# Performance work log

Hardware: AMD Instinct MI355X
Metric: run time of the kernel (lower is better)

The kernel has to match this reference:

```python
import jax, jax.numpy as jnp
import numpy as np

HIDDEN_DIM = 1024
NUM_HEADS = 16
HEAD_DIM = HIDDEN_DIM // NUM_HEADS
ROPE_BASE = 10000.0


def setup_inputs() -> dict:
    key = jax.random.key(0)
    kx, kq, kk, kv, ko = jax.random.split(key, 5)
    B, S = 2, 2048
    scale = 1.0 / np.sqrt(HIDDEN_DIM)
    x = jax.random.normal(kx, (B, S, HIDDEN_DIM), dtype=jnp.float32)
    Wq = jax.random.normal(kq, (HIDDEN_DIM, HIDDEN_DIM), dtype=jnp.float32) * scale
    Wk = jax.random.normal(kk, (HIDDEN_DIM, HIDDEN_DIM), dtype=jnp.float32) * scale
    Wv = jax.random.normal(kv, (HIDDEN_DIM, HIDDEN_DIM), dtype=jnp.float32) * scale
    Wo = jax.random.normal(ko, (HIDDEN_DIM, HIDDEN_DIM), dtype=jnp.float32) * scale
    return {"x": x, "Wq": Wq, "Wk": Wk, "Wv": Wv, "Wo": Wo}


def _apply_rope(t, positions):
    # t: (B, S, H, D), positions: (B, S)
    half = HEAD_DIM // 2
    inv_freq = 1.0 / (ROPE_BASE ** (jnp.arange(0, half, dtype=jnp.float32) * 2.0 / HEAD_DIM))
    freqs = positions[..., None].astype(jnp.float32) * inv_freq  # (B, S, D/2)
    emb = jnp.concatenate([freqs, freqs], axis=-1)  # (B, S, D)
    cos = jnp.cos(emb)[:, :, None, :]
    sin = jnp.sin(emb)[:, :, None, :]
    t1, t2 = t[..., :half], t[..., half:]
    rot = jnp.concatenate([-t2, t1], axis=-1)
    return t * cos + rot * sin


def reference(x, Wq, Wk, Wv, Wo):
    B, S, _ = x.shape
    H, D = NUM_HEADS, HEAD_DIM
    q = (x @ Wq.T).reshape(B, S, H, D)
    k = (x @ Wk.T).reshape(B, S, H, D)
    v = (x @ Wv.T).reshape(B, S, H, D)
    positions = jnp.broadcast_to(jnp.arange(S)[None, :], (B, S))
    q = _apply_rope(q, positions)
    k = _apply_rope(k, positions)
    # SDPA (non-causal, no mask): scores (B, H, S, S)
    scale = 1.0 / np.sqrt(D)
    scores = jnp.einsum('bqhd,bkhd->bhqk', q, k) * scale
    probs = jax.nn.softmax(scores, axis=-1)
    out = jnp.einsum('bhqk,bkhd->bqhd', probs, v).reshape(B, S, H * D)
    return out @ Wo.T
```

## Files before the change

kernel.cpp:

```cpp
#include <hip/hip_runtime.h>


typedef unsigned short u16;
typedef unsigned int   u32;
typedef __bf16 bf16x8 __attribute__((ext_vector_type(8)));
typedef float  f32x4  __attribute__((ext_vector_type(4)));
typedef u16    u16x8  __attribute__((ext_vector_type(8)));
typedef u16    u16x4  __attribute__((ext_vector_type(4)));
typedef u32    u32x4  __attribute__((ext_vector_type(4)));

#define HID 1024
#define SEQ 2048
#define NH  16
#define HD  64

#if __has_builtin(__builtin_amdgcn_exp2f)
#define EXP2F(x) __builtin_amdgcn_exp2f(x)
#else
#define EXP2F(x) exp2f(x)
#endif

__device__ __forceinline__ float bf2f(u16 u) { return __uint_as_float(((unsigned)u) << 16); }
__device__ __forceinline__ u16 f2bf(float f) {
  union { __bf16 h; u16 u; } c;
  c.h = (__bf16)f;
  return c.u;
}
__device__ __forceinline__ void gl_lds16(const void* g, void* l) {
  __builtin_amdgcn_global_load_lds((const __attribute__((address_space(1))) void*)g,
                                   (__attribute__((address_space(3))) void*)l, 16, 0, 0);
}
__device__ __forceinline__ void stage_f32(const float* __restrict__ src, u16* dst) {
  float4 f0 = *(const float4*)src;
  float4 f1 = *(const float4*)(src + 4);
  u16x8 o;
  o[0] = f2bf(f0.x); o[1] = f2bf(f0.y); o[2] = f2bf(f0.z); o[3] = f2bf(f0.w);
  o[4] = f2bf(f1.x); o[5] = f2bf(f1.y); o[6] = f2bf(f1.z); o[7] = f2bf(f1.w);
  *(u16x8*)dst = o;
}
__device__ __forceinline__ int swz(int c, int r) { return c ^ (r & 7); }

__global__ void cvt_pre(const float* __restrict__ x,  const float* __restrict__ Wq,
                        const float* __restrict__ Wk, const float* __restrict__ Wv,
                        u16* __restrict__ xb, u16* __restrict__ Wqb,
                        u16* __restrict__ Wkb, u16* __restrict__ Wvb) {
  const int z = blockIdx.y;
  const float* src; u16* dst; int nchunk;
  switch (z) {
    case 0:  src = x;  dst = xb;  nchunk = 524288; break;
    case 1:  src = Wq; dst = Wqb; nchunk = 131072; break;
    case 2:  src = Wk; dst = Wkb; nchunk = 131072; break;
    default: src = Wv; dst = Wvb; nchunk = 131072; break;
  }
  const int i = blockIdx.x * 256 + threadIdx.x;
  if (i >= nchunk) return;
  stage_f32(src + (size_t)i * 8, dst + (size_t)i * 8);
}
__global__ void cvt_wo(const float* __restrict__ Wo, u16* __restrict__ Wob) {
  const int i = blockIdx.x * 256 + threadIdx.x;
  stage_f32(Wo + (size_t)i * 8, Wob + (size_t)i * 8);
}

__device__ __forceinline__ void gemm_mainloop(const u16* __restrict__ Aptr,
                                              const u16* __restrict__ Bptr,
                                              u16* a_lds, u16* b_lds,
                                              int m0, int n0, f32x4 (&acc)[4][4]) {
  const int tid  = threadIdx.x;
  const int w    = tid >> 6;
  const int lane = tid & 63;
  const int quad = lane >> 4, l15 = lane & 15;
  const int wm = (w >> 1) * 64, wn = (w & 1) * 64;
  const int srow = lane >> 3, sc = lane & 7;

  for (int k0 = 0; k0 < HID; k0 += 64) {
#pragma unroll
    for (int i = 0; i < 4; ++i) {
      const int seg = w * 4 + i;
      const int r   = seg * 8 + srow;
      const int col = k0 + swz(sc, srow) * 8;
      gl_lds16(Aptr + (size_t)(m0 + r) * HID + col, a_lds + seg * 512);
      gl_lds16(Bptr + (size_t)(n0 + r) * HID + col, b_lds + seg * 512);
    }
    __syncthreads();
#pragma unroll
    for (int kf = 0; kf < 2; ++kf) {
      bf16x8 af[4], bfr[4];
#pragma unroll
      for (int mt = 0; mt < 4; ++mt)
        af[mt] = *(const bf16x8*)&a_lds[(wm + mt * 16 + l15) * 64 + swz(kf * 4 + quad, l15) * 8];
#pragma unroll
      for (int nt = 0; nt < 4; ++nt)
        bfr[nt] = *(const bf16x8*)&b_lds[(wn + nt * 16 + l15) * 64 + swz(kf * 4 + quad, l15) * 8];
#pragma unroll
      for (int mt = 0; mt < 4; ++mt)
#pragma unroll
        for (int nt = 0; nt < 4; ++nt)
          acc[mt][nt] = __builtin_amdgcn_mfma_f32_16x16x32_bf16(af[mt], bfr[nt], acc[mt][nt], 0, 0, 0);
    }
    __syncthreads();
  }
}

__device__ __forceinline__ void gemm64_mainloop(const u16* __restrict__ Aptr,
                                                const u16* __restrict__ Bptr,
                                                u16* a_lds, u16* b_lds,
                                                int m0, int n0, f32x4 (&acc)[2][4]) {
  const int tid  = threadIdx.x;
  const int w    = tid >> 6;
  const int lane = tid & 63;
  const int quad = lane >> 4, l15 = lane & 15;
  const int wm = (w >> 1) * 32, wn = (w & 1) * 64;
  const int srow = lane >> 3, sc = lane & 7;

  for (int k0 = 0; k0 < HID; k0 += 64) {
#pragma unroll
    for (int i = 0; i < 2; ++i) {
      const int seg = w * 2 + i, r = seg * 8 + srow;
      gl_lds16(Aptr + (size_t)(m0 + r) * HID + k0 + swz(sc, srow) * 8, a_lds + seg * 512);
    }
#pragma unroll
    for (int i = 0; i < 4; ++i) {
      const int seg = w * 4 + i, r = seg * 8 + srow;
      gl_lds16(Bptr + (size_t)(n0 + r) * HID + k0 + swz(sc, srow) * 8, b_lds + seg * 512);
    }
    __syncthreads();
#pragma unroll
    for (int kf = 0; kf < 2; ++kf) {
      bf16x8 af[2], bfr[4];
#pragma unroll
      for (int mt = 0; mt < 2; ++mt)
        af[mt] = *(const bf16x8*)&a_lds[(wm + mt * 16 + l15) * 64 + swz(kf * 4 + quad, l15) * 8];
#pragma unroll
      for (int nt = 0; nt < 4; ++nt)
        bfr[nt] = *(const bf16x8*)&b_lds[(wn + nt * 16 + l15) * 64 + swz(kf * 4 + quad, l15) * 8];
#pragma unroll
      for (int mt = 0; mt < 2; ++mt)
#pragma unroll
        for (int nt = 0; nt < 4; ++nt)
          acc[mt][nt] = __builtin_amdgcn_mfma_f32_16x16x32_bf16(af[mt], bfr[nt], acc[mt][nt], 0, 0, 0);
    }
    __syncthreads();
  }
}

#define QS_LOG2E 0.18033688011112042f
__global__ __launch_bounds__(256, 2) void qkv_gemm(const u16* __restrict__ xb,
                                                   const u16* __restrict__ Wqb,
                                                   const u16* __restrict__ Wkb,
                                                   const u16* __restrict__ Wvb,
                                                   u16* __restrict__ q, u16* __restrict__ k,
                                                   u16* __restrict__ vT) {
  __shared__ __align__(16) u16 a_lds[128 * 64];
  __shared__ __align__(16) u16 b_lds[128 * 64];
  const int z = blockIdx.z;
  const u16* W = (z == 0) ? Wqb : (z == 1) ? Wkb : Wvb;

  f32x4 acc[4][4];
#pragma unroll
  for (int i = 0; i < 4; ++i)
#pragma unroll
    for (int j = 0; j < 4; ++j) acc[i][j] = (f32x4){0.f, 0.f, 0.f, 0.f};

  const int m0 = blockIdx.x * 128, n0 = blockIdx.y * 128;
  gemm_mainloop(xb, W, a_lds, b_lds, m0, n0, acc);

  const int tid = threadIdx.x, w = tid >> 6, lane = tid & 63;
  const int quad = lane >> 4, l15 = lane & 15;
  const int wm = (w >> 1) * 64, wn = (w & 1) * 64;

  if (z != 2) {
    float fr[2];
    fr[0] = __expf(-(float)(l15)      * 0.2878231366242557f);
    fr[1] = __expf(-(float)(16 + l15) * 0.2878231366242557f);
    const float qs = (z == 0) ? QS_LOG2E : 1.f;
#pragma unroll
    for (int mt = 0; mt < 4; ++mt)
#pragma unroll
      for (int r = 0; r < 4; ++r) {
        const int s = (m0 + wm + mt * 16 + quad * 4 + r) & 2047;
#pragma unroll
        for (int p = 0; p < 2; ++p) {
          float c, sn;
          __sincosf((float)s * fr[p], &sn, &c);
          const float t1 = acc[mt][p][r], t2 = acc[mt][p + 2][r];
          acc[mt][p][r]     = (t1 * c - t2 * sn) * qs;
          acc[mt][p + 2][r] = (t2 * c + t1 * sn) * qs;
        }
      }
    u16* dst = (z == 0) ? q : k;
#pragma unroll
    for (int mt = 0; mt < 4; ++mt)
#pragma unroll
      for (int nt = 0; nt < 4; ++nt) {
        const int col = n0 + wn + nt * 16 + l15;
        const int h = col >> 6, d = col & 63;
#pragma unroll
        for (int r = 0; r < 4; ++r) {
          const int row = m0 + wm + mt * 16 + quad * 4 + r;
          const int bh  = (row >> 11) * NH + h;
          dst[((size_t)bh * SEQ + (row & 2047)) * HD + d] = f2bf(acc[mt][nt][r]);
        }
      }
  } else {
#pragma unroll
    for (int mt = 0; mt < 4; ++mt) {
      const int rowbase = m0 + wm + mt * 16 + quad * 4;
      const int b = rowbase >> 11, s0 = rowbase & 2047;
#pragma unroll
      for (int nt = 0; nt < 4; ++nt) {
        const int col = n0 + wn + nt * 16 + l15;
        const int h = col >> 6, d = col & 63;
        u16x4 o;
#pragma unroll
        for (int r = 0; r < 4; ++r) o[r] = f2bf(acc[mt][nt][r]);
        *(u16x4*)&vT[((size_t)(b * NH + h) * HD + d) * SEQ + s0] = o;
      }
    }
  }
}

__global__ __launch_bounds__(256, 2) void flash(const u16* __restrict__ q,
                                                const u16* __restrict__ k,
                                                const u16* __restrict__ vT,
                                                u16* __restrict__ attn) {
  __shared__ __align__(16) u16 ktl[2 * 4096];
  __shared__ __align__(16) u16 vtl[2 * 4096];

  const int tid = threadIdx.x, w = tid >> 6, lane = tid & 63;
  const int quad = lane >> 4, l15 = lane & 15;
  const int srow = lane >> 3, sc = lane & 7;
  const int bh = blockIdx.x;
  const int q0 = blockIdx.y * 128;

  const u16* kbase = k  + (size_t)bh * SEQ * HD;
  const u16* vtb   = vT + (size_t)bh * HD * SEQ;

  bf16x8 qa[2][2];
#pragma unroll
  for (int qh = 0; qh < 2; ++qh) {
    const u16* qrow = q + ((size_t)bh * SEQ + q0 + w * 32 + qh * 16 + l15) * HD + quad * 8;
    qa[qh][0] = *(const bf16x8*)qrow;
    qa[qh][1] = *(const bf16x8*)(qrow + 32);
  }

  const int colsw = swz(sc, srow) * 8;
#define ISSUE(T, B) do {                                                                  \
    _Pragma("unroll")                                                                     \
    for (int i = 0; i < 2; ++i) {                                                         \
      const int seg = w * 2 + i, r = seg * 8 + srow;                                      \
      gl_lds16(kbase + (size_t)((T) * 64 + r) * HD + colsw, &ktl[(B) * 4096 + seg * 512]); \
      gl_lds16(vtb + (size_t)r * SEQ + (T) * 64 + colsw,    &vtl[(B) * 4096 + seg * 512]); \
    } } while (0)

  const f32x4 zero4 = (f32x4){0.f, 0.f, 0.f, 0.f};
  f32x4 oacc[2][4];
#pragma unroll
  for (int qh = 0; qh < 2; ++qh)
#pragma unroll
    for (int i = 0; i < 4; ++i) oacc[qh][i] = zero4;
  float L[2] = {0.f, 0.f};

  ISSUE(0, 0);
  __syncthreads();

  for (int t = 0; t < 32; ++t) {
    const int buf = t & 1;
    if (t < 31) ISSUE(t + 1, buf ^ 1);

    const u16* kc = &ktl[buf * 4096];
    const u16* vc = &vtl[buf * 4096];
    bf16x8 kfr[2][4], bvf[2][4];
#pragma unroll
    for (int kf = 0; kf < 2; ++kf)
#pragma unroll
      for (int nt = 0; nt < 4; ++nt) {
        kfr[kf][nt] = *(const bf16x8*)&kc[(nt * 16 + l15) * 64 + swz(kf * 4 + quad, l15) * 8];
        bvf[kf][nt] = *(const bf16x8*)&vc[(nt * 16 + l15) * 64 + swz(kf * 4 + quad, l15) * 8];
      }

    __builtin_amdgcn_s_setprio(1);
#pragma unroll
    for (int qh = 0; qh < 2; ++qh) {
      f32x4 sv[4];
#pragma unroll
      for (int nt = 0; nt < 4; ++nt) {
        sv[nt] = __builtin_amdgcn_mfma_f32_16x16x32_bf16(kfr[0][nt], qa[qh][0], zero4, 0, 0, 0);
        sv[nt] = __builtin_amdgcn_mfma_f32_16x16x32_bf16(kfr[1][nt], qa[qh][1], sv[nt], 0, 0, 0);
      }
      u32 pd[4][2];
#pragma unroll
      for (int nt = 0; nt < 4; ++nt)
#pragma unroll
        for (int e = 0; e < 2; ++e) {
          const float p0 = EXP2F(sv[nt][2 * e]);
          const float p1 = EXP2F(sv[nt][2 * e + 1]);
          L[qh] += p0 + p1;
          asm("v_cvt_pk_bf16_f32 %0, %1, %2" : "=v"(pd[nt][e]) : "v"(p0), "v"(p1));
        }
#pragma unroll
      for (int kf = 0; kf < 2; ++kf) {
        u32 a0 = pd[2 * kf][0], b0 = pd[2 * kf + 1][0];
        u32 a1 = pd[2 * kf][1], b1 = pd[2 * kf + 1][1];
        asm("v_permlane32_swap_b32 %0, %1" : "+v"(a0), "+v"(b0));
        asm("v_permlane32_swap_b32 %0, %1" : "+v"(a1), "+v"(b1));
        asm("v_permlane16_swap_b32 %0, %1" : "+v"(a0), "+v"(b0));
        asm("v_permlane16_swap_b32 %0, %1" : "+v"(a1), "+v"(b1));
        const u32x4 apw = (u32x4){a0, a1, b0, b1};
        const bf16x8 ap = __builtin_bit_cast(bf16x8, apw);
#pragma unroll
        for (int dt = 0; dt < 4; ++dt)
          oacc[qh][dt] = __builtin_amdgcn_mfma_f32_16x16x32_bf16(ap, bvf[kf][dt], oacc[qh][dt], 0, 0, 0);
      }
    }
    __builtin_amdgcn_s_setprio(0);
    __syncthreads();
  }
#undef ISSUE

  const int b = bh >> 4, h = bh & 15;
#pragma unroll
  for (int qh = 0; qh < 2; ++qh) {
    float Lf = L[qh];
    Lf += __shfl_xor(Lf, 16, 64);
    Lf += __shfl_xor(Lf, 32, 64);
    float inv[4];
#pragma unroll
    for (int r = 0; r < 4; ++r) inv[r] = 1.f / __shfl(Lf, quad * 4 + r, 64);
#pragma unroll
    for (int r = 0; r < 4; ++r) {
      const int row = b * SEQ + q0 + w * 32 + qh * 16 + quad * 4 + r;
#pragma unroll
      for (int dt = 0; dt < 4; ++dt)
        attn[(size_t)row * HID + h * HD + dt * 16 + l15] = f2bf(oacc[qh][dt][r] * inv[r]);
    }
  }
}

__global__ __launch_bounds__(256, 4) void out_gemm(const u16* __restrict__ attn,
                                                   const u16* __restrict__ Wob,
                                                   float* __restrict__ out) {
  __shared__ __align__(16) u16 a_lds[64 * 64];
  __shared__ __align__(16) u16 b_lds[128 * 64];
  f32x4 acc[2][4];
#pragma unroll
  for (int i = 0; i < 2; ++i)
#pragma unroll
    for (int j = 0; j < 4; ++j) acc[i][j] = (f32x4){0.f, 0.f, 0.f, 0.f};

  const int m0 = blockIdx.x * 64, n0 = blockIdx.y * 128;
  gemm64_mainloop(attn, Wob, a_lds, b_lds, m0, n0, acc);

  const int tid = threadIdx.x, w = tid >> 6, lane = tid & 63;
  const int quad = lane >> 4, l15 = lane & 15;
  const int wm = (w >> 1) * 32, wn = (w & 1) * 64;
#pragma unroll
  for (int mt = 0; mt < 2; ++mt)
#pragma unroll
    for (int nt = 0; nt < 4; ++nt) {
      const int col = n0 + wn + nt * 16 + l15;
#pragma unroll
      for (int r = 0; r < 4; ++r) {
        const int row = m0 + wm + mt * 16 + quad * 4 + r;
        out[(size_t)row * HID + col] = acc[mt][nt][r];
      }
    }
}

extern "C" void kernel_launch(void* const* d_in, const int* in_sizes, int n_in,
                              void* d_out, int out_size, void* d_ws, size_t ws_size,
                              hipStream_t stream) {
  const float* x  = (const float*)d_in[0];
  const float* Wq = (const float*)d_in[1];
  const float* Wk = (const float*)d_in[2];
  const float* Wv = (const float*)d_in[3];
  const float* Wo = (const float*)d_in[4];
  float* out = (float*)d_out;

  char* os = (char*)d_out;
  u16* Wqb = (u16*)(os);
  u16* Wkb = (u16*)(os + (2u << 20));
  u16* Wvb = (u16*)(os + (4u << 20));
  u16* xb  = (u16*)(os + (6u << 20));

  char* ws = (char*)d_ws;
  u16* q    = (u16*)(ws);
  u16* Wob  = (u16*)(ws);
  u16* k    = (u16*)(ws + (8u << 20));
  u16* vT   = (u16*)(ws + (16u << 20));
  u16* attn = (u16*)(ws + (24u << 20));

  cvt_pre<<<dim3(2048, 4), 256, 0, stream>>>(x, Wq, Wk, Wv, xb, Wqb, Wkb, Wvb);
  qkv_gemm<<<dim3(32, 8, 3), 256, 0, stream>>>(xb, Wqb, Wkb, Wvb, q, k, vT);
  flash<<<dim3(32, 16), 256, 0, stream>>>(q, k, vT, attn);
  cvt_wo<<<dim3(512), 256, 0, stream>>>(Wo, Wob);
  out_gemm<<<dim3(64, 8), 256, 0, stream>>>(attn, Wob, out);
}
```

Measured before the change: 174.1 us.

## Load K/V fragments directly from global into registers, dropping LDS staging

The flash kernel no longer stages K and V^T tiles through double-buffered shared memory with barriers. Each lane now loads its MFMA fragments straight from global memory into registers, with a software pipeline that alternates two K register sets and prefetches the next tile while computing. This removes LDS traffic and __syncthreads, but every wave now reads K/V from global/L2 on its own (four times the reads per block) and needs more registers, which may lower occupancy.

```diff
diff --git a/kernel.cpp b/kernel.cpp
--- a/kernel.cpp
+++ b/kernel.cpp
@@ -223,17 +223,13 @@
                                                 const u16* __restrict__ k,
                                                 const u16* __restrict__ vT,
                                                 u16* __restrict__ attn) {
-  __shared__ __align__(16) u16 ktl[2 * 4096];
-  __shared__ __align__(16) u16 vtl[2 * 4096];
-
   const int tid = threadIdx.x, w = tid >> 6, lane = tid & 63;
   const int quad = lane >> 4, l15 = lane & 15;
-  const int srow = lane >> 3, sc = lane & 7;
   const int bh = blockIdx.x;
   const int q0 = blockIdx.y * 128;
 
-  const u16* kbase = k  + (size_t)bh * SEQ * HD;
-  const u16* vtb   = vT + (size_t)bh * HD * SEQ;
+  const u16* kfl = k  + (size_t)bh * SEQ * HD + (size_t)l15 * HD + quad * 8;
+  const u16* vfl = vT + (size_t)bh * HD * SEQ + (size_t)l15 * SEQ + quad * 8;
 
   bf16x8 qa[2][2];
 #pragma unroll
@@ -243,15 +239,6 @@
     qa[qh][1] = *(const bf16x8*)(qrow + 32);
   }
 
-  const int colsw = swz(sc, srow) * 8;
-#define ISSUE(T, B) do {                                                                  \
-    _Pragma("unroll")                                                                     \
-    for (int i = 0; i < 2; ++i) {                                                         \
-      const int seg = w * 2 + i, r = seg * 8 + srow;                                      \
-      gl_lds16(kbase + (size_t)((T) * 64 + r) * HD + colsw, &ktl[(B) * 4096 + seg * 512]); \
-      gl_lds16(vtb + (size_t)r * SEQ + (T) * 64 + colsw,    &vtl[(B) * 4096 + seg * 512]); \
-    } } while (0)
-
   const f32x4 zero4 = (f32x4){0.f, 0.f, 0.f, 0.f};
   f32x4 oacc[2][4];
 #pragma unroll
@@ -260,62 +247,73 @@
     for (int i = 0; i < 4; ++i) oacc[qh][i] = zero4;
   float L[2] = {0.f, 0.f};
 
-  ISSUE(0, 0);
-  __syncthreads();
-
-  for (int t = 0; t < 32; ++t) {
-    const int buf = t & 1;
-    if (t < 31) ISSUE(t + 1, buf ^ 1);
-
-    const u16* kc = &ktl[buf * 4096];
-    const u16* vc = &vtl[buf * 4096];
-    bf16x8 kfr[2][4], bvf[2][4];
-#pragma unroll
-    for (int kf = 0; kf < 2; ++kf)
-#pragma unroll
-      for (int nt = 0; nt < 4; ++nt) {
-        kfr[kf][nt] = *(const bf16x8*)&kc[(nt * 16 + l15) * 64 + swz(kf * 4 + quad, l15) * 8];
-        bvf[kf][nt] = *(const bf16x8*)&vc[(nt * 16 + l15) * 64 + swz(kf * 4 + quad, l15) * 8];
-      }
-
-    __builtin_amdgcn_s_setprio(1);
-#pragma unroll
-    for (int qh = 0; qh < 2; ++qh) {
-      f32x4 sv[4];
-#pragma unroll
-      for (int nt = 0; nt < 4; ++nt) {
-        sv[nt] = __builtin_amdgcn_mfma_f32_16x16x32_bf16(kfr[0][nt], qa[qh][0], zero4, 0, 0, 0);
-        sv[nt] = __builtin_amdgcn_mfma_f32_16x16x32_bf16(kfr[1][nt], qa[qh][1], sv[nt], 0, 0, 0);
-      }
-      u32 pd[4][2];
-#pragma unroll
-      for (int nt = 0; nt < 4; ++nt)
-#pragma unroll
-        for (int e = 0; e < 2; ++e) {
-          const float p0 = EXP2F(sv[nt][2 * e]);
-          const float p1 = EXP2F(sv[nt][2 * e + 1]);
-          L[qh] += p0 + p1;
-          asm("v_cvt_pk_bf16_f32 %0, %1, %2" : "=v"(pd[nt][e]) : "v"(p0), "v"(p1));
-        }
-#pragma unroll
-      for (int kf = 0; kf < 2; ++kf) {
-        u32 a0 = pd[2 * kf][0], b0 = pd[2 * kf + 1][0];
-        u32 a1 = pd[2 * kf][1], b1 = pd[2 * kf + 1][1];
-        asm("v_permlane32_swap_b32 %0, %1" : "+v"(a0), "+v"(b0));
-        asm("v_permlane32_swap_b32 %0, %1" : "+v"(a1), "+v"(b1));
-        asm("v_permlane16_swap_b32 %0, %1" : "+v"(a0), "+v"(b0));
-        asm("v_permlane16_swap_b32 %0, %1" : "+v"(a1), "+v"(b1));
-        const u32x4 apw = (u32x4){a0, a1, b0, b1};
-        const bf16x8 ap = __builtin_bit_cast(bf16x8, apw);
-#pragma unroll
-        for (int dt = 0; dt < 4; ++dt)
-          oacc[qh][dt] = __builtin_amdgcn_mfma_f32_16x16x32_bf16(ap, bvf[kf][dt], oacc[qh][dt], 0, 0, 0);
-      }
-    }
-    __builtin_amdgcn_s_setprio(0);
-    __syncthreads();
-  }
-#undef ISSUE
+  bf16x8 kA[2][4], kB[2][4], vV[2][4];
+
+#define LOADK(DST, T) do {                                                         \
+    _Pragma("unroll")                                                              \
+    for (int kf = 0; kf < 2; ++kf)                                                 \
+      _Pragma("unroll")                                                            \
+      for (int nt = 0; nt < 4; ++nt)                                               \
+        DST[kf][nt] = *(const bf16x8*)&kfl[(size_t)((T) * 64 + nt * 16) * HD + kf * 32]; \
+  } while (0)
+#define LOADV(T) do {                                                              \
+    _Pragma("unroll")                                                              \
+    for (int kf = 0; kf < 2; ++kf)                                                 \
+      _Pragma("unroll")                                                            \
+      for (int nt = 0; nt < 4; ++nt)                                               \
+        vV[kf][nt] = *(const bf16x8*)&vfl[(size_t)(nt * 16) * SEQ + (T) * 64 + kf * 32]; \
+  } while (0)
+
+#define COMPUTE(KF) do {                                                           \
+    __builtin_amdgcn_s_setprio(1);                                                 \
+    _Pragma("unroll")                                                              \
+    for (int qh = 0; qh < 2; ++qh) {                                               \
+      f32x4 sv[4];                                                                 \
+      _Pragma("unroll")                                                            \
+      for (int nt = 0; nt < 4; ++nt) {                                             \
+        sv[nt] = __builtin_amdgcn_mfma_f32_16x16x32_bf16(KF[0][nt], qa[qh][0], zero4, 0, 0, 0); \
+        sv[nt] = __builtin_amdgcn_mfma_f32_16x16x32_bf16(KF[1][nt], qa[qh][1], sv[nt], 0, 0, 0); \
+      }                                                                            \
+      u32 pd[4][2];                                                                \
+      _Pragma("unroll")                                                            \
+      for (int nt = 0; nt < 4; ++nt)                                               \
+        _Pragma("unroll")                                                          \
+        for (int e = 0; e < 2; ++e) {                                              \
+          const float p0 = EXP2F(sv[nt][2 * e]);                                   \
+          const float p1 = EXP2F(sv[nt][2 * e + 1]);                               \
+          L[qh] += p0 + p1;                                                        \
+          asm("v_cvt_pk_bf16_f32 %0, %1, %2" : "=v"(pd[nt][e]) : "v"(p0), "v"(p1)); \
+        }                                                                          \
+      _Pragma("unroll")                                                            \
+      for (int kf = 0; kf < 2; ++kf) {                                             \
+        u32 a0 = pd[2 * kf][0], b0 = pd[2 * kf + 1][0];                            \
+        u32 a1 = pd[2 * kf][1], b1 = pd[2 * kf + 1][1];                            \
+        asm("v_permlane32_swap_b32 %0, %1" : "+v"(a0), "+v"(b0));                  \
+        asm("v_permlane32_swap_b32 %0, %1" : "+v"(a1), "+v"(b1));                  \
+        asm("v_permlane16_swap_b32 %0, %1" : "+v"(a0), "+v"(b0));                  \
+        asm("v_permlane16_swap_b32 %0, %1" : "+v"(a1), "+v"(b1));                  \
+        const u32x4 apw = (u32x4){a0, a1, b0, b1};                                 \
+        const bf16x8 ap = __builtin_bit_cast(bf16x8, apw);                         \
+        _Pragma("unroll")                                                          \
+        for (int dt = 0; dt < 4; ++dt)                                             \
+          oacc[qh][dt] = __builtin_amdgcn_mfma_f32_16x16x32_bf16(ap, vV[kf][dt], oacc[qh][dt], 0, 0, 0); \
+      }                                                                            \
+    }                                                                              \
+    __builtin_amdgcn_s_setprio(0);                                                 \
+  } while (0)
+
+  LOADK(kA, 0);
+  for (int t = 0; t < 32; t += 2) {
+    LOADV(t);
+    LOADK(kB, t + 1);
+    COMPUTE(kA);
+    LOADV(t + 1);
+    if (t + 2 < 32) LOADK(kA, t + 2);
+    COMPUTE(kB);
+  }
+#undef LOADK
+#undef LOADV
+#undef COMPUTE
 
   const int b = bh >> 4, h = bh & 15;
 #pragma unroll
```

New measurement: 246.0 us. 41.3% more time.
